# Kernel tuning notes

Hardware: AMD Instinct MI355X
Metric: run time of the kernel (lower is better)

## Reference

```python
import jax, jax.numpy as jnp
import numpy as np

B, S, D = 4, 4096, 768  # batch, seq_len, n_units
NEG = -1000000000.0      # masked_fill value from the torch source


def setup_inputs() -> dict:
    key = jax.random.key(0)
    ks = jax.random.split(key, 12)
    scale = 1.0 / np.sqrt(D)
    inp = {
        "query": jax.random.normal(ks[0], (B, S, D), jnp.float32),
        "key_": jax.random.normal(ks[1], (B, S, D), jnp.float32),
        "value": jax.random.normal(ks[2], (B, S, D), jnp.float32),
        # nn.Linear weights are [out, in]; forward computes x @ W.T + b
        "Wq": jax.random.normal(ks[3], (D, D), jnp.float32) * scale,
        "bq": jnp.zeros((D,), jnp.float32),
        "Wk": jax.random.normal(ks[4], (D, D), jnp.float32) * scale,
        "bk": jnp.zeros((D,), jnp.float32),
        "Wv": jax.random.normal(ks[5], (D, D), jnp.float32) * scale,
        "bv": jnp.zeros((D,), jnp.float32),
        "Wo": jax.random.normal(ks[6], (D, D), jnp.float32) * scale,
        "bo": jnp.zeros((D,), jnp.float32),
        # broadcastable causal mask [1, S, S]; 0 -> masked
        "mask": jnp.tril(jnp.ones((S, S), jnp.int32))[None, :, :],
    }
    return inp


def reference(query, key_, value, Wq, bq, Wk, bk, Wv, bv, Wo, bo, mask):
    # QKV projections (torch Linear: x @ W.T + b)
    q = jnp.einsum("bsd,ed->bse", query, Wq) + bq
    k = jnp.einsum("bsd,ed->bse", key_, Wk) + bk
    v = jnp.einsum("bsd,ed->bse", value, Wv) + bv
    # scores: NOTE source scales by n_units**0.5 (full model dim, no head split)
    weights = jnp.einsum("bqd,bkd->bqk", q, k) / jnp.sqrt(jnp.float32(D))
    weights = jnp.where(mask == 0, jnp.float32(NEG), weights)
    weights = jax.nn.softmax(weights, axis=-1)
    # dropout is identity in eval/deterministic reference
    attended = jnp.einsum("bqk,bkd->bqd", weights, v)
    return jnp.einsum("bsd,ed->bse", attended, Wo) + bo
```

## Files before the change

kernel.cpp:

```cpp
#include <hip/hip_runtime.h>
#include <hip/hip_bf16.h>
#include <stdint.h>

#define DI __device__ __forceinline__

typedef __bf16 bf16x4 __attribute__((ext_vector_type(4)));
typedef __bf16 bf16x8 __attribute__((ext_vector_type(8)));
typedef float  f32x4  __attribute__((ext_vector_type(4)));

static constexpr int  BATCH = 4;
static constexpr int  SEQ   = 4096;
static constexpr int  DIM   = 768;
static constexpr long TOK   = (long)BATCH * SEQ;
static constexpr int  QT    = SEQ / 128;
static constexpr int  NTRI  = QT * (QT + 1) / 2;
static constexpr float SCALE = 0.0360843918243516150f;

__global__ void cvt3_kernel(const float* __restrict__ a, const float* __restrict__ b,
                            const float* __restrict__ c, __bf16* __restrict__ oa,
                            __bf16* __restrict__ ob, __bf16* __restrict__ oc, long n4){
  const float* in  = blockIdx.y == 0 ? a : blockIdx.y == 1 ? b : c;
  __bf16*      out = blockIdx.y == 0 ? oa : blockIdx.y == 1 ? ob : oc;
  long i = (long)blockIdx.x * blockDim.x + threadIdx.x;
  const long stride = (long)gridDim.x * blockDim.x;
  for(; i < n4; i += stride){
    float4 v = ((const float4*)in)[i];
    bf16x4 o = { (__bf16)v.x, (__bf16)v.y, (__bf16)v.z, (__bf16)v.w };
    ((bf16x4*)out)[i] = o;
  }
}
__global__ void cvt4_kernel(const float* __restrict__ a, const float* __restrict__ b,
                            const float* __restrict__ c, const float* __restrict__ d,
                            __bf16* __restrict__ oa, __bf16* __restrict__ ob,
                            __bf16* __restrict__ oc, __bf16* __restrict__ od, long n4){
  const float* in  = blockIdx.y == 0 ? a : blockIdx.y == 1 ? b : blockIdx.y == 2 ? c : d;
  __bf16*      out = blockIdx.y == 0 ? oa : blockIdx.y == 1 ? ob : blockIdx.y == 2 ? oc : od;
  long i = (long)blockIdx.x * blockDim.x + threadIdx.x;
  const long stride = (long)gridDim.x * blockDim.x;
  for(; i < n4; i += stride){
    float4 v = ((const float4*)in)[i];
    bf16x4 o = { (__bf16)v.x, (__bf16)v.y, (__bf16)v.z, (__bf16)v.w };
    ((bf16x4*)out)[i] = o;
  }
}

DI int swz_off(int r, int c){ return (r << 7) + ((c ^ (r & 7)) << 4); }

template<int NT, int R>
DI void stage(const __bf16* __restrict__ src, long ld, char* lds, int tid){
  const int w = tid >> 6, l = tid & 63;
  const int rsub = l >> 3;
  const int kc   = (l & 7) ^ rsub;
  const __bf16* g = src + (long)(w * 8 + rsub) * ld + kc * 8;
  char* d = lds + (w << 10);
  constexpr int RPC = (NT / 64) * 8;
  #pragma unroll
  for(int i = 0; i < R / RPC; ++i){
    __builtin_amdgcn_global_load_lds(
        (const __attribute__((address_space(1))) void*)(g + (long)(i * RPC) * ld),
        (__attribute__((address_space(3))) void*)(d + i * RPC * 128), 16, 0, 0);
  }
}

DI bf16x8 frag_ld(const char* lds, int row, int c){
  return *(const bf16x8*)(lds + swz_off(row, c));
}

DI void mma_tile(const char* As, const char* Bs, int lane, int wr, int wc, f32x4 acc[4][4]){
  #pragma unroll
  for(int kk = 0; kk < 2; ++kk){
    const int c = kk * 4 + (lane >> 4);
    bf16x8 a[4], b[4];
    #pragma unroll
    for(int i = 0; i < 4; ++i) a[i] = frag_ld(As, wr + i * 16 + (lane & 15), c);
    #pragma unroll
    for(int j = 0; j < 4; ++j) b[j] = frag_ld(Bs, wc + j * 16 + (lane & 15), c);
    #pragma unroll
    for(int i = 0; i < 4; ++i)
      #pragma unroll
      for(int j = 0; j < 4; ++j)
        acc[i][j] = __builtin_amdgcn_mfma_f32_16x16x32_bf16(a[i], b[j], acc[i][j], 0, 0, 0);
  }
}

template<bool OUTF32, bool BIASM>
__global__ __launch_bounds__(512)
void gemm256_bt(const __bf16* __restrict__ A, const __bf16* __restrict__ B,
                const float* __restrict__ bias, void* __restrict__ C,
                int K, long lda, long ldb, long ldc){
  __shared__ __attribute__((aligned(128))) char As[16384];
  __shared__ __attribute__((aligned(128))) char Bs[32768];
  const int tid = threadIdx.x, lane = tid & 63, w = tid >> 6;
  const int wr = (w >> 2) * 64, wc = (w & 3) * 64;
  const long m0 = (long)blockIdx.y * 128, n0 = (long)blockIdx.x * 256;
  f32x4 acc[4][4] = {};
  for(int k0 = 0; k0 < K; k0 += 64){
    stage<512, 128>(A + m0 * lda + k0, lda, As, tid);
    stage<512, 256>(B + n0 * ldb + k0, ldb, Bs, tid);
    __syncthreads();
    mma_tile(As, Bs, lane, wr, wc, acc);
    __syncthreads();
  }
  const int cl = lane & 15, rq = (lane >> 4) * 4;
  #pragma unroll
  for(int i = 0; i < 4; ++i)
    #pragma unroll
    for(int j = 0; j < 4; ++j){
      const long gc = n0 + wc + j * 16 + cl;
      #pragma unroll
      for(int e = 0; e < 4; ++e){
        const long gr = m0 + wr + i * 16 + rq + e;
        float v = acc[i][j][e] + (BIASM ? bias[gr] : bias[gc]);
        if(OUTF32) ((float*)C)[gr * ldc + gc] = v;
        else       ((__bf16*)C)[gr * ldc + gc] = (__bf16)v;
      }
    }
}

__global__ __launch_bounds__(512)
void qk_kernel(const __bf16* __restrict__ qb, const __bf16* __restrict__ kb,
               __bf16* __restrict__ Pc){
  const int b = blockIdx.y;
  const int t2 = blockIdx.x;
  int Qi = (int)((sqrtf(4.0f * t2 + 1.0f) - 1.0f) * 0.5f);
  while((Qi + 1) * (Qi + 2) <= t2) Qi++;
  while(Qi * (Qi + 1) > t2) Qi--;
  const int ki = t2 - Qi * (Qi + 1);
  const __bf16* Aq = qb + ((long)b * SEQ + Qi * 256) * DIM;
  const __bf16* Bk = kb + ((long)b * SEQ + ki * 128) * DIM;
  __shared__ __attribute__((aligned(128))) char As[32768];
  __shared__ __attribute__((aligned(128))) char Bs[16384];
  const int tid = threadIdx.x, lane = tid & 63, w = tid >> 6;
  const int wr = (w >> 1) * 64, wc = (w & 1) * 64;
  f32x4 acc[4][4] = {};
  for(int k0 = 0; k0 < DIM; k0 += 64){
    stage<512, 256>(Aq + k0, DIM, As, tid);
    stage<512, 128>(Bk + k0, DIM, Bs, tid);
    __syncthreads();
    mma_tile(As, Bs, lane, wr, wc, acc);
    __syncthreads();
  }
  const int cl = lane & 15, rq = (lane >> 4) * 4;
  #pragma unroll
  for(int i = 0; i < 4; ++i){
    const int rbase = wr + i * 16;
    const int qi = 2 * Qi + (rbase >> 7);
    if(ki > qi) continue;
    const bool diag = (ki == qi);
    __bf16* tile = Pc + ((long)b * NTRI + (long)qi * (qi + 1) / 2 + ki) * 16384;
    #pragma unroll
    for(int j = 0; j < 4; ++j){
      const int c = wc + j * 16 + cl;
      #pragma unroll
      for(int e = 0; e < 4; ++e){
        const int rloc = (rbase + rq + e) & 127;
        float p = (diag && c > rloc) ? 0.0f
                  : __expf(fminf(acc[i][j][e] * SCALE, 30.0f));
        tile[rloc * 128 + c] = (__bf16)p;
      }
    }
  }
}

__global__ void rowsum(const __bf16* __restrict__ Pc, float* __restrict__ rlrow){
  const int gr = blockIdx.x * 4 + (threadIdx.x >> 6);
  const int lane = threadIdx.x & 63;
  const int b = gr >> 12, r = gr & 4095;
  const int qi = r >> 7, rloc = r & 127;
  const __bf16* base = Pc + ((long)b * NTRI + (long)qi * (qi + 1) / 2) * 16384
                       + rloc * 128;
  float s = 0.f;
  for(int ki = 0; ki <= qi; ++ki){
    uint32_t u = *(const uint32_t*)(base + (long)ki * 16384 + lane * 2);
    s += __uint_as_float(u << 16) + __uint_as_float(u & 0xffff0000u);
  }
  #pragma unroll
  for(int off = 32; off; off >>= 1) s += __shfl_xor(s, off);
  if(lane == 0) rlrow[gr] = 1.0f / s;
}

__global__ __launch_bounds__(512)
void pv_kernel(const __bf16* __restrict__ Pc, const float* __restrict__ rlrow,
               const __bf16* __restrict__ vbT, __bf16* __restrict__ att){
  const int b = blockIdx.z, qi = 31 - blockIdx.y;
  const long n0 = (long)blockIdx.x * 256;
  __shared__ __attribute__((aligned(128))) char As[16384];
  __shared__ __attribute__((aligned(128))) char Bs[32768];
  __shared__ float sRl[128];
  const int tid = threadIdx.x, lane = tid & 63, w = tid >> 6;
  const int wr = (w >> 2) * 64, wc = (w & 3) * 64;
  if(tid < 128) sRl[tid] = rlrow[b * SEQ + qi * 128 + tid];
  f32x4 acc[4][4] = {};
  const __bf16* Pq = Pc + ((long)b * NTRI + (long)qi * (qi + 1) / 2) * 16384;
  const __bf16* Bv = vbT + n0 * TOK + (long)b * SEQ;
  __syncthreads();
  for(int kt = 0; kt <= qi; ++kt){
    #pragma unroll
    for(int half = 0; half < 2; ++half){
      stage<512, 128>(Pq + (long)kt * 16384 + half * 64, 128, As, tid);
      stage<512, 256>(Bv + (long)kt * 128 + half * 64, TOK, Bs, tid);
      __syncthreads();
      mma_tile(As, Bs, lane, wr, wc, acc);
      __syncthreads();
    }
  }
  const int cl = lane & 15, rq = (lane >> 4) * 4;
  #pragma unroll
  for(int i = 0; i < 4; ++i)
    #pragma unroll
    for(int j = 0; j < 4; ++j){
      const long gc = n0 + wc + j * 16 + cl;
      #pragma unroll
      for(int e = 0; e < 4; ++e){
        const int rloc = wr + i * 16 + rq + e;
        float v = acc[i][j][e] * sRl[rloc];
        att[((long)b * SEQ + qi * 128 + rloc) * DIM + gc] = (__bf16)v;
      }
    }
}

extern "C" void kernel_launch(void* const* d_in, const int* in_sizes, int n_in,
                              void* d_out, int out_size, void* d_ws, size_t ws_size,
                              hipStream_t stream){
  const float* query = (const float*)d_in[0];
  const float* key_  = (const float*)d_in[1];
  const float* value = (const float*)d_in[2];
  const float* Wq = (const float*)d_in[3];
  const float* bq = (const float*)d_in[4];
  const float* Wk = (const float*)d_in[5];
  const float* bk = (const float*)d_in[6];
  const float* Wv = (const float*)d_in[7];
  const float* bv = (const float*)d_in[8];
  const float* Wo = (const float*)d_in[9];
  const float* bo = (const float*)d_in[10];

  char* p = (char*)d_ws;
  auto carve = [&](size_t bytes)->char*{
    char* r = p; p += (bytes + 255) & ~(size_t)255; return r;
  };
  const size_t tb = (size_t)TOK * DIM * 2;
  __bf16* xq  = (__bf16*)carve(tb);
  __bf16* xk  = (__bf16*)carve(tb);
  __bf16* xv  = (__bf16*)carve(tb);
  __bf16* qb  = (__bf16*)carve(tb);
  __bf16* kb  = (__bf16*)carve(tb);
  __bf16* vbT = (__bf16*)carve(tb);
  __bf16* Wqb = (__bf16*)carve((size_t)DIM * DIM * 2);
  __bf16* Wkb = (__bf16*)carve((size_t)DIM * DIM * 2);
  __bf16* Wvb = (__bf16*)carve((size_t)DIM * DIM * 2);
  __bf16* Wob = (__bf16*)carve((size_t)DIM * DIM * 2);
  __bf16* Pc  = (__bf16*)carve((size_t)BATCH * NTRI * 16384 * 2);
  float*  rlr = (float*)carve((size_t)TOK * 4);
  __bf16* att = xq;
  if((size_t)(p - (char*)d_ws) > ws_size) return;

  const long nIn4 = TOK * DIM / 4, nW4 = (long)DIM * DIM / 4;
  dim3 g3(2048, 3), g4((unsigned)((nW4 + 255) / 256), 4);
  cvt3_kernel<<<g3, 256, 0, stream>>>(query, key_, value, xq, xk, xv, nIn4);
  cvt4_kernel<<<g4, 256, 0, stream>>>(Wq, Wk, Wv, Wo, Wqb, Wkb, Wvb, Wob, nW4);

  dim3 gProj(DIM / 256, TOK / 128);
  gemm256_bt<false, false><<<gProj, 512, 0, stream>>>(xq, Wqb, bq, qb, DIM, DIM, DIM, DIM);
  gemm256_bt<false, false><<<gProj, 512, 0, stream>>>(xk, Wkb, bk, kb, DIM, DIM, DIM, DIM);
  dim3 gVT(TOK / 256, DIM / 128);
  gemm256_bt<false, true><<<gVT, 512, 0, stream>>>(Wvb, xv, bv, vbT, DIM, DIM, DIM, TOK);

  dim3 gQK(272, BATCH);
  qk_kernel<<<gQK, 512, 0, stream>>>(qb, kb, Pc);

  rowsum<<<TOK / 4, 256, 0, stream>>>(Pc, rlr);

  dim3 gPV(DIM / 256, QT, BATCH);
  pv_kernel<<<gPV, 512, 0, stream>>>(Pc, rlr, vbT, att);

  gemm256_bt<true, false><<<gProj, 512, 0, stream>>>(att, Wob, bo, d_out, DIM, DIM, DIM, DIM);
}
```

Before: 329.1 us.

## Triple-buffer GEMM k-loops, fuse QKV projections, fold rowsum into PV kernel

Replaces the single-buffered GEMM loop with a shared triple-buffered kloop that prefetches two tiles ahead with partial vmcnt waits and raises wave priority around the MFMA block. The three projection launches are merged into one kernel. The QK tile shape changes to 128 query rows by 256 key columns. The separate rowsum kernel is removed: the PV kernel sums the P fragments it already loads from LDS. The goal is to hide global-to-LDS latency, cut launch count, and skip a full extra pass over the P matrix, at the cost of 144KB of LDS per block, which limits occupancy to one block per CU.

```diff
diff --git a/kernel.cpp b/kernel.cpp
--- a/kernel.cpp
+++ b/kernel.cpp
@@ -46,19 +46,18 @@
 
 DI int swz_off(int r, int c){ return (r << 7) + ((c ^ (r & 7)) << 4); }
 
-template<int NT, int R>
+template<int R>
 DI void stage(const __bf16* __restrict__ src, long ld, char* lds, int tid){
   const int w = tid >> 6, l = tid & 63;
   const int rsub = l >> 3;
   const int kc   = (l & 7) ^ rsub;
   const __bf16* g = src + (long)(w * 8 + rsub) * ld + kc * 8;
   char* d = lds + (w << 10);
-  constexpr int RPC = (NT / 64) * 8;
-  #pragma unroll
-  for(int i = 0; i < R / RPC; ++i){
+  #pragma unroll
+  for(int i = 0; i < R / 64; ++i){
     __builtin_amdgcn_global_load_lds(
-        (const __attribute__((address_space(1))) void*)(g + (long)(i * RPC) * ld),
-        (__attribute__((address_space(3))) void*)(d + i * RPC * 128), 16, 0, 0);
+        (const __attribute__((address_space(1))) void*)(g + (long)(i * 64) * ld),
+        (__attribute__((address_space(3))) void*)(d + i * 8192), 16, 0, 0);
   }
 }
 
@@ -66,41 +65,70 @@
   return *(const bf16x8*)(lds + swz_off(row, c));
 }
 
-DI void mma_tile(const char* As, const char* Bs, int lane, int wr, int wc, f32x4 acc[4][4]){
-  #pragma unroll
-  for(int kk = 0; kk < 2; ++kk){
-    const int c = kk * 4 + (lane >> 4);
-    bf16x8 a[4], b[4];
-    #pragma unroll
-    for(int i = 0; i < 4; ++i) a[i] = frag_ld(As, wr + i * 16 + (lane & 15), c);
-    #pragma unroll
-    for(int j = 0; j < 4; ++j) b[j] = frag_ld(Bs, wc + j * 16 + (lane & 15), c);
-    #pragma unroll
-    for(int i = 0; i < 4; ++i)
+template<bool SUMA>
+DI void mma_phase(const char* As, const char* Bs, int lane, int wr, int wc, int kk,
+                  f32x4 acc[4][4], float* rs){
+  const int c = kk * 4 + (lane >> 4);
+  bf16x8 a[4], b[4];
+  #pragma unroll
+  for(int i = 0; i < 4; ++i) a[i] = frag_ld(As, wr + i * 16 + (lane & 15), c);
+  #pragma unroll
+  for(int j = 0; j < 4; ++j) b[j] = frag_ld(Bs, wc + j * 16 + (lane & 15), c);
+  __builtin_amdgcn_s_setprio(1);
+  #pragma unroll
+  for(int i = 0; i < 4; ++i)
+    #pragma unroll
+    for(int j = 0; j < 4; ++j)
+      acc[i][j] = __builtin_amdgcn_mfma_f32_16x16x32_bf16(a[i], b[j], acc[i][j], 0, 0, 0);
+  __builtin_amdgcn_s_setprio(0);
+  if(SUMA){
+    #pragma unroll
+    for(int i = 0; i < 4; ++i){
+      float s = 0.f;
       #pragma unroll
-      for(int j = 0; j < 4; ++j)
-        acc[i][j] = __builtin_amdgcn_mfma_f32_16x16x32_bf16(a[i], b[j], acc[i][j], 0, 0, 0);
-  }
-}
-
-template<bool OUTF32, bool BIASM>
-__global__ __launch_bounds__(512)
-void gemm256_bt(const __bf16* __restrict__ A, const __bf16* __restrict__ B,
-                const float* __restrict__ bias, void* __restrict__ C,
-                int K, long lda, long ldb, long ldc){
-  __shared__ __attribute__((aligned(128))) char As[16384];
-  __shared__ __attribute__((aligned(128))) char Bs[32768];
-  const int tid = threadIdx.x, lane = tid & 63, w = tid >> 6;
+      for(int e = 0; e < 8; ++e) s += (float)a[i][e];
+      rs[i] += s;
+    }
+  }
+}
+
+template<bool SUM, class FA, class FB>
+DI void kloop(FA fa, long lda, FB fb, long ldb, int nt, int tid,
+              char* As, char* Bs, f32x4 acc[4][4], float* rs){
+  const int lane = tid & 63, w = tid >> 6;
   const int wr = (w >> 2) * 64, wc = (w & 3) * 64;
-  const long m0 = (long)blockIdx.y * 128, n0 = (long)blockIdx.x * 256;
-  f32x4 acc[4][4] = {};
-  for(int k0 = 0; k0 < K; k0 += 64){
-    stage<512, 128>(A + m0 * lda + k0, lda, As, tid);
-    stage<512, 256>(B + n0 * ldb + k0, ldb, Bs, tid);
-    __syncthreads();
-    mma_tile(As, Bs, lane, wr, wc, acc);
-    __syncthreads();
-  }
+  stage<128>(fa(0), lda, As, tid);
+  stage<256>(fb(0), ldb, Bs, tid);
+  if(nt > 1){
+    stage<128>(fa(1), lda, As + 16384, tid);
+    stage<256>(fb(1), ldb, Bs + 32768, tid);
+  }
+  int buf = 0;
+  for(int t = 0; t < nt; ++t){
+    if(t + 1 < nt) asm volatile("s_waitcnt vmcnt(6)" ::: "memory");
+    else           asm volatile("s_waitcnt vmcnt(0)" ::: "memory");
+    __builtin_amdgcn_s_barrier();
+    const char* Ab = As + buf * 16384;
+    const char* Bb = Bs + buf * 32768;
+    const int pbuf = buf == 0 ? 2 : buf - 1;
+    const bool pf = (t + 2 < nt);
+    if(pf) stage<128>(fa(t + 2), lda, As + pbuf * 16384, tid);
+    if(SUM && wc == 0) mma_phase<true >(Ab, Bb, lane, wr, wc, 0, acc, rs);
+    else               mma_phase<false>(Ab, Bb, lane, wr, wc, 0, acc, rs);
+    if(pf) stage<256>(fb(t + 2), ldb, Bs + pbuf * 32768, tid);
+    if(SUM && wc == 0) mma_phase<true >(Ab, Bb, lane, wr, wc, 1, acc, rs);
+    else               mma_phase<false>(Ab, Bb, lane, wr, wc, 1, acc, rs);
+    asm volatile("" ::: "memory");
+    __builtin_amdgcn_s_barrier();
+    buf = buf == 2 ? 0 : buf + 1;
+  }
+}
+
+template<bool OUTF32>
+DI void epi_store(f32x4 acc[4][4], const float* bias, bool biasm, void* C,
+                  long m0, long n0, long ldc, int tid){
+  const int lane = tid & 63, w = tid >> 6;
+  const int wr = (w >> 2) * 64, wc = (w & 3) * 64;
   const int cl = lane & 15, rq = (lane >> 4) * 4;
   #pragma unroll
   for(int i = 0; i < 4; ++i)
@@ -110,7 +138,7 @@
       #pragma unroll
       for(int e = 0; e < 4; ++e){
         const long gr = m0 + wr + i * 16 + rq + e;
-        float v = acc[i][j][e] + (BIASM ? bias[gr] : bias[gc]);
+        float v = acc[i][j][e] + bias[biasm ? gr : gc];
         if(OUTF32) ((float*)C)[gr * ldc + gc] = v;
         else       ((__bf16*)C)[gr * ldc + gc] = (__bf16)v;
       }
@@ -118,92 +146,118 @@
 }
 
 __global__ __launch_bounds__(512)
+void proj_qkv(const __bf16* __restrict__ xq, const __bf16* __restrict__ xk,
+              const __bf16* __restrict__ xv, const __bf16* __restrict__ Wqb,
+              const __bf16* __restrict__ Wkb, const __bf16* __restrict__ Wvb,
+              const float* __restrict__ bq, const float* __restrict__ bk,
+              const float* __restrict__ bv, __bf16* __restrict__ qb,
+              __bf16* __restrict__ kb, __bf16* __restrict__ vbT){
+  __shared__ __attribute__((aligned(128))) char As[49152];
+  __shared__ __attribute__((aligned(128))) char Bs[98304];
+  const int z = blockIdx.y, bid = blockIdx.x, tid = threadIdx.x;
+  const __bf16 *A, *B; const float* bias; __bf16* C;
+  long m0, n0, ldc; bool biasm;
+  if(z == 0){ A = xq;  B = Wqb; bias = bq; C = qb;
+              n0 = (bid % 3) * 256; m0 = (bid / 3) * 128; ldc = DIM; biasm = false; }
+  else if(z == 1){ A = xk;  B = Wkb; bias = bk; C = kb;
+              n0 = (bid % 3) * 256; m0 = (bid / 3) * 128; ldc = DIM; biasm = false; }
+  else {      A = Wvb; B = xv;  bias = bv; C = vbT;
+              n0 = (bid % 64) * 256; m0 = (bid / 64) * 128; ldc = TOK; biasm = true; }
+  const __bf16* Ar = A + m0 * DIM;
+  const __bf16* Br = B + n0 * DIM;
+  f32x4 acc[4][4] = {};
+  auto fa = [&](int t){ return Ar + t * 64; };
+  auto fb = [&](int t){ return Br + t * 64; };
+  kloop<false>(fa, DIM, fb, DIM, DIM / 64, tid, As, Bs, acc, nullptr);
+  epi_store<false>(acc, bias, biasm, C, m0, n0, ldc, tid);
+}
+
+__global__ __launch_bounds__(512)
+void oproj(const __bf16* __restrict__ att, const __bf16* __restrict__ Wob,
+           const float* __restrict__ bo, float* __restrict__ out){
+  __shared__ __attribute__((aligned(128))) char As[49152];
+  __shared__ __attribute__((aligned(128))) char Bs[98304];
+  const int bid = blockIdx.x, tid = threadIdx.x;
+  const long n0 = (bid % 3) * 256, m0 = (long)(bid / 3) * 128;
+  const __bf16* Ar = att + m0 * DIM;
+  const __bf16* Br = Wob + n0 * DIM;
+  f32x4 acc[4][4] = {};
+  auto fa = [&](int t){ return Ar + t * 64; };
+  auto fb = [&](int t){ return Br + t * 64; };
+  kloop<false>(fa, DIM, fb, DIM, DIM / 64, tid, As, Bs, acc, nullptr);
+  epi_store<true>(acc, bo, false, out, m0, n0, DIM, tid);
+}
+
+__global__ __launch_bounds__(512)
 void qk_kernel(const __bf16* __restrict__ qb, const __bf16* __restrict__ kb,
                __bf16* __restrict__ Pc){
-  const int b = blockIdx.y;
-  const int t2 = blockIdx.x;
-  int Qi = (int)((sqrtf(4.0f * t2 + 1.0f) - 1.0f) * 0.5f);
-  while((Qi + 1) * (Qi + 2) <= t2) Qi++;
-  while(Qi * (Qi + 1) > t2) Qi--;
-  const int ki = t2 - Qi * (Qi + 1);
-  const __bf16* Aq = qb + ((long)b * SEQ + Qi * 256) * DIM;
-  const __bf16* Bk = kb + ((long)b * SEQ + ki * 128) * DIM;
-  __shared__ __attribute__((aligned(128))) char As[32768];
-  __shared__ __attribute__((aligned(128))) char Bs[16384];
-  const int tid = threadIdx.x, lane = tid & 63, w = tid >> 6;
-  const int wr = (w >> 1) * 64, wc = (w & 1) * 64;
+  __shared__ __attribute__((aligned(128))) char As[49152];
+  __shared__ __attribute__((aligned(128))) char Bs[98304];
+  const int b = blockIdx.y, t2 = blockIdx.x, tid = threadIdx.x;
+  int m = (int)((sqrtf(4.0f * t2 + 1.0f) - 1.0f) * 0.5f);
+  while((m + 1) * (m + 2) <= t2) ++m;
+  while(m * (m + 1) > t2) --m;
+  int qi, Kp;
+  if(t2 < (m + 1) * (m + 1)){ qi = 2 * m;     Kp = t2 - m * (m + 1); }
+  else                      { qi = 2 * m + 1; Kp = t2 - (m + 1) * (m + 1); }
+  const __bf16* Aq = qb + ((long)b * SEQ + qi * 128) * DIM;
+  const __bf16* Bk = kb + ((long)b * SEQ + Kp * 256) * DIM;
   f32x4 acc[4][4] = {};
-  for(int k0 = 0; k0 < DIM; k0 += 64){
-    stage<512, 256>(Aq + k0, DIM, As, tid);
-    stage<512, 128>(Bk + k0, DIM, Bs, tid);
-    __syncthreads();
-    mma_tile(As, Bs, lane, wr, wc, acc);
-    __syncthreads();
-  }
+  auto fa = [&](int t){ return Aq + t * 64; };
+  auto fb = [&](int t){ return Bk + t * 64; };
+  kloop<false>(fa, DIM, fb, DIM, DIM / 64, tid, As, Bs, acc, nullptr);
+
+  const int lane = tid & 63, w = tid >> 6;
+  const int wr = (w >> 2) * 64, wc = (w & 3) * 64;
   const int cl = lane & 15, rq = (lane >> 4) * 4;
   #pragma unroll
-  for(int i = 0; i < 4; ++i){
-    const int rbase = wr + i * 16;
-    const int qi = 2 * Qi + (rbase >> 7);
+  for(int j = 0; j < 4; ++j){
+    const int ki = 2 * Kp + ((wc + j * 16) >> 7);
     if(ki > qi) continue;
     const bool diag = (ki == qi);
     __bf16* tile = Pc + ((long)b * NTRI + (long)qi * (qi + 1) / 2 + ki) * 16384;
-    #pragma unroll
-    for(int j = 0; j < 4; ++j){
-      const int c = wc + j * 16 + cl;
+    const int kcol = ((wc + j * 16) & 127) + cl;
+    #pragma unroll
+    for(int i = 0; i < 4; ++i){
       #pragma unroll
       for(int e = 0; e < 4; ++e){
-        const int rloc = (rbase + rq + e) & 127;
-        float p = (diag && c > rloc) ? 0.0f
+        const int rloc = wr + i * 16 + rq + e;
+        float p = (diag && kcol > rloc) ? 0.0f
                   : __expf(fminf(acc[i][j][e] * SCALE, 30.0f));
-        tile[rloc * 128 + c] = (__bf16)p;
+        tile[rloc * 128 + kcol] = (__bf16)p;
       }
     }
   }
 }
 
-__global__ void rowsum(const __bf16* __restrict__ Pc, float* __restrict__ rlrow){
-  const int gr = blockIdx.x * 4 + (threadIdx.x >> 6);
-  const int lane = threadIdx.x & 63;
-  const int b = gr >> 12, r = gr & 4095;
-  const int qi = r >> 7, rloc = r & 127;
-  const __bf16* base = Pc + ((long)b * NTRI + (long)qi * (qi + 1) / 2) * 16384
-                       + rloc * 128;
-  float s = 0.f;
-  for(int ki = 0; ki <= qi; ++ki){
-    uint32_t u = *(const uint32_t*)(base + (long)ki * 16384 + lane * 2);
-    s += __uint_as_float(u << 16) + __uint_as_float(u & 0xffff0000u);
-  }
-  #pragma unroll
-  for(int off = 32; off; off >>= 1) s += __shfl_xor(s, off);
-  if(lane == 0) rlrow[gr] = 1.0f / s;
-}
-
 __global__ __launch_bounds__(512)
-void pv_kernel(const __bf16* __restrict__ Pc, const float* __restrict__ rlrow,
-               const __bf16* __restrict__ vbT, __bf16* __restrict__ att){
-  const int b = blockIdx.z, qi = 31 - blockIdx.y;
+void pv_kernel(const __bf16* __restrict__ Pc, const __bf16* __restrict__ vbT,
+               __bf16* __restrict__ att){
+  __shared__ __attribute__((aligned(128))) char As[49152];
+  __shared__ __attribute__((aligned(128))) char Bs[98304];
+  __shared__ float sInv[128];
+  const int b = blockIdx.z, qi = 31 - blockIdx.y, tid = threadIdx.x;
   const long n0 = (long)blockIdx.x * 256;
-  __shared__ __attribute__((aligned(128))) char As[16384];
-  __shared__ __attribute__((aligned(128))) char Bs[32768];
-  __shared__ float sRl[128];
-  const int tid = threadIdx.x, lane = tid & 63, w = tid >> 6;
-  const int wr = (w >> 2) * 64, wc = (w & 3) * 64;
-  if(tid < 128) sRl[tid] = rlrow[b * SEQ + qi * 128 + tid];
-  f32x4 acc[4][4] = {};
   const __bf16* Pq = Pc + ((long)b * NTRI + (long)qi * (qi + 1) / 2) * 16384;
   const __bf16* Bv = vbT + n0 * TOK + (long)b * SEQ;
+  f32x4 acc[4][4] = {};
+  float rs[4] = {0.f, 0.f, 0.f, 0.f};
+  auto fa = [&](int t){ return Pq + (long)(t >> 1) * 16384 + (t & 1) * 64; };
+  auto fb = [&](int t){ return Bv + t * 64; };
+  kloop<true>(fa, 128, fb, TOK, 2 * (qi + 1), tid, As, Bs, acc, rs);
+
+  const int lane = tid & 63, w = tid >> 6;
+  const int wr = (w >> 2) * 64, wc = (w & 3) * 64;
+  if(wc == 0){
+    #pragma unroll
+    for(int i = 0; i < 4; ++i){
+      float s = rs[i];
+      s += __shfl_xor(s, 16);
+      s += __shfl_xor(s, 32);
+      if(lane < 16) sInv[wr + i * 16 + lane] = 1.0f / s;
+    }
+  }
   __syncthreads();
-  for(int kt = 0; kt <= qi; ++kt){
-    #pragma unroll
-    for(int half = 0; half < 2; ++half){
-      stage<512, 128>(Pq + (long)kt * 16384 + half * 64, 128, As, tid);
-      stage<512, 256>(Bv + (long)kt * 128 + half * 64, TOK, Bs, tid);
-      __syncthreads();
-      mma_tile(As, Bs, lane, wr, wc, acc);
-      __syncthreads();
-    }
-  }
   const int cl = lane & 15, rq = (lane >> 4) * 4;
   #pragma unroll
   for(int i = 0; i < 4; ++i)
@@ -213,7 +267,7 @@
       #pragma unroll
       for(int e = 0; e < 4; ++e){
         const int rloc = wr + i * 16 + rq + e;
-        float v = acc[i][j][e] * sRl[rloc];
+        float v = acc[i][j][e] * sInv[rloc];
         att[((long)b * SEQ + qi * 128 + rloc) * DIM + gc] = (__bf16)v;
       }
     }
@@ -250,7 +304,6 @@
   __bf16* Wvb = (__bf16*)carve((size_t)DIM * DIM * 2);
   __bf16* Wob = (__bf16*)carve((size_t)DIM * DIM * 2);
   __bf16* Pc  = (__bf16*)carve((size_t)BATCH * NTRI * 16384 * 2);
-  float*  rlr = (float*)carve((size_t)TOK * 4);
   __bf16* att = xq;
   if((size_t)(p - (char*)d_ws) > ws_size) return;
 
@@ -259,19 +312,12 @@
   cvt3_kernel<<<g3, 256, 0, stream>>>(query, key_, value, xq, xk, xv, nIn4);
   cvt4_kernel<<<g4, 256, 0, stream>>>(Wq, Wk, Wv, Wo, Wqb, Wkb, Wvb, Wob, nW4);
 
-  dim3 gProj(DIM / 256, TOK / 128);
-  gemm256_bt<false, false><<<gProj, 512, 0, stream>>>(xq, Wqb, bq, qb, DIM, DIM, DIM, DIM);
-  gemm256_bt<false, false><<<gProj, 512, 0, stream>>>(xk, Wkb, bk, kb, DIM, DIM, DIM, DIM);
-  dim3 gVT(TOK / 256, DIM / 128);
-  gemm256_bt<false, true><<<gVT, 512, 0, stream>>>(Wvb, xv, bv, vbT, DIM, DIM, DIM, TOK);
-
-  dim3 gQK(272, BATCH);
-  qk_kernel<<<gQK, 512, 0, stream>>>(qb, kb, Pc);
-
-  rowsum<<<TOK / 4, 256, 0, stream>>>(Pc, rlr);
-
-  dim3 gPV(DIM / 256, QT, BATCH);
-  pv_kernel<<<gPV, 512, 0, stream>>>(Pc, rlr, vbT, att);
-
-  gemm256_bt<true, false><<<gProj, 512, 0, stream>>>(att, Wob, bo, d_out, DIM, DIM, DIM, DIM);
-}
+  proj_qkv<<<dim3(384, 3), 512, 0, stream>>>(xq, xk, xv, Wqb, Wkb, Wvb,
+                                             bq, bk, bv, qb, kb, vbT);
+
+  qk_kernel<<<dim3(272, BATCH), 512, 0, stream>>>(qb, kb, Pc);
+
+  pv_kernel<<<dim3(3, QT, BATCH), 512, 0, stream>>>(Pc, vbT, att);
+
+  oproj<<<384, 512, 0, stream>>>(att, Wob, bo, (float*)d_out);
+}
```

After: 390.1 us. 1.19x slower.
